# Performance work log

Measured on AMD Instinct MI355X. Metric: run time of the kernel, lower is better.

Reference implementation:

```python
import jax, jax.numpy as jnp
import numpy as np

TOPK_FRAC = 0.2

def _l2norm(v, eps=1e-12):
    return v / (jnp.linalg.norm(v) + eps)

def _spectral_normalize(w, u):
    # torch.nn.utils.spectral_norm forward: one power iteration (u,v detached),
    # sigma = u^T W v with gradient flowing through W only.
    wm = w.reshape(w.shape[0], -1)            # (out, in*kh*kw)
    v = _l2norm(jax.lax.stop_gradient(wm).T @ u)
    u_new = _l2norm(jax.lax.stop_gradient(wm) @ v)
    sigma = jnp.einsum('i,ij,j->', u_new, wm, v)
    return w / sigma

def setup_inputs() -> dict:
    key = jax.random.key(0)
    ks = jax.random.split(key, 5)
    N, C, H, W = 32, 512, 56, 56
    return {
        'x':  jax.random.normal(ks[0], (N, C, H, W), dtype=jnp.float32),
        'w1': jax.random.normal(ks[1], (C, C, 4, 4), dtype=jnp.float32) * 0.05,
        'w2': jax.random.normal(ks[2], (C, C, 1, 1), dtype=jnp.float32) * 0.05,
        'u1': jax.random.normal(ks[3], (C,), dtype=jnp.float32),
        'u2': jax.random.normal(ks[4], (C,), dtype=jnp.float32),
    }

def reference(x, w1, w2, u1, u2):
    N, C, H, W = x.shape
    # AdaptiveAvgPool2d(4): H,W divisible by 4 -> uniform 14x14 windows
    p = x.reshape(N, C, 4, H // 4, 4, W // 4).mean(axis=(3, 5))   # (N,C,4,4)
    p = jax.nn.sigmoid(p)
    # spectral-norm conv 4x4, valid, no bias -> fully reduces spatial to 1x1
    w1n = _spectral_normalize(w1, u1)                             # (C,C,4,4)
    h = jnp.einsum('ncij,ocij->no', p, w1n)                       # (N,C)
    h = jax.nn.relu(h)
    # spectral-norm conv 1x1
    w2n = _spectral_normalize(w2, u2).reshape(C, C)               # (out,in)
    s = jax.nn.sigmoid(jnp.einsum('nc,oc->no', h, w2n))           # (N,C)
    # sparse_ch: keep top int(0.2*C) channels per sample
    k = int(max(1, TOPK_FRAC * C))
    _, idx = jax.lax.top_k(s, k)                                  # (N,k)
    mask = jnp.zeros_like(s).at[jnp.arange(N)[:, None], idx].set(1.0)
    weight = (s * mask)[:, :, None, None]                         # (N,C,1,1)
    return x * weight
```

## Files before the change

kernel.cpp:

```cpp
#include <hip/hip_runtime.h>


#define KTOP 102

__device__ __forceinline__ float block_sum256(float v) {
  __shared__ float red[4];
  #pragma unroll
  for (int off = 32; off; off >>= 1) v += __shfl_down(v, off, 64);
  int lane = threadIdx.x & 63;
  int w = threadIdx.x >> 6;
  if (lane == 0) red[w] = v;
  __syncthreads();
  float r = 0.f;
  if (threadIdx.x == 0) r = red[0] + red[1] + red[2] + red[3];
  return r;
}

__global__ __launch_bounds__(256) void k_pool(const float* __restrict__ x, float* __restrict__ p) {
  __shared__ float sx[3136];
  int plane = blockIdx.x;
  const float* xp = x + (size_t)plane * 3136;
  for (int e = threadIdx.x; e < 3136; e += 256) sx[e] = xp[e];
  __syncthreads();
  int t = threadIdx.x;
  int w = t >> 4, lane = t & 15;
  int wr = w >> 2, wc = w & 3;
  float acc = 0.f;
  for (int e = lane; e < 196; e += 16) {
    int r = e / 14, cc = e - r * 14;
    acc += sx[(14 * wr + r) * 56 + 14 * wc + cc];
  }
  #pragma unroll
  for (int off = 8; off; off >>= 1) acc += __shfl_down(acc, off, 16);
  if (lane == 0) {
    float m = acc * (1.f / 196.f);
    p[(size_t)plane * 16 + w] = 1.f / (1.f + expf(-m));
  }
}

__global__ __launch_bounds__(256) void k_sn1(const float* __restrict__ w1, const float* __restrict__ w2,
                                             const float* __restrict__ u1, const float* __restrict__ u2,
                                             float* __restrict__ part1, float* __restrict__ part1b) {
  __shared__ float su[64];
  int b = blockIdx.x, t = threadIdx.x;
  if (b < 256) {
    int jb = b & 31, ic = b >> 5;
    if (t < 64) su[t] = u1[ic * 64 + t];
    __syncthreads();
    int j = jb * 256 + t;
    const float* base = w1 + (size_t)(ic * 64) * 8192 + j;
    float acc = 0.f;
    #pragma unroll 4
    for (int i = 0; i < 64; ++i) acc += base[(size_t)i * 8192] * su[i];
    part1[ic * 8192 + j] = acc;
  } else {
    int bb = b - 256;
    int jb = bb & 1, ic = bb >> 1;
    if (t < 64) su[t] = u2[ic * 64 + t];
    __syncthreads();
    int j = jb * 256 + t;
    const float* base = w2 + (size_t)(ic * 64) * 512 + j;
    float acc = 0.f;
    #pragma unroll 4
    for (int i = 0; i < 64; ++i) acc += base[(size_t)i * 512] * su[i];
    part1b[ic * 512 + j] = acc;
  }
}

__global__ __launch_bounds__(256) void k_sn1r(const float* __restrict__ part1, const float* __restrict__ part1b,
                                              float* __restrict__ t1, float* __restrict__ t1b,
                                              float* __restrict__ scal) {
  int b = blockIdx.x, t = threadIdx.x;
  float s = 0.f;
  if (b < 32) {
    int j = b * 256 + t;
    #pragma unroll
    for (int ic = 0; ic < 8; ++ic) s += part1[ic * 8192 + j];
    t1[j] = s;
    float tot = block_sum256(s * s);
    if (t == 0) atomicAdd(&scal[0], tot);
  } else {
    int j = (b - 32) * 256 + t;
    #pragma unroll
    for (int ic = 0; ic < 8; ++ic) s += part1b[ic * 512 + j];
    t1b[j] = s;
    float tot = block_sum256(s * s);
    if (t == 0) atomicAdd(&scal[1], tot);
  }
}

__global__ __launch_bounds__(256) void k_sn2(const float* __restrict__ w1, const float* __restrict__ w2,
                                             const float* __restrict__ t1, const float* __restrict__ t1b,
                                             float* __restrict__ scal) {
  int b = blockIdx.x, t = threadIdx.x;
  if (b < 512) {
    float inv = 1.f / (sqrtf(scal[0]) + 1e-12f);
    const float4* row = (const float4*)(w1 + (size_t)b * 8192);
    const float4* tv = (const float4*)t1;
    float acc = 0.f;
    for (int q = t; q < 2048; q += 256) {
      float4 a = row[q], v = tv[q];
      acc += a.x * v.x + a.y * v.y + a.z * v.z + a.w * v.w;
    }
    float tot = block_sum256(acc);
    if (t == 0) { float r = tot * inv; atomicAdd(&scal[2], r * r); }
  } else {
    int i = b - 512;
    float inv = 1.f / (sqrtf(scal[1]) + 1e-12f);
    const float4* row = (const float4*)(w2 + (size_t)i * 512);
    const float4* tv = (const float4*)t1b;
    float acc = 0.f;
    if (t < 128) {
      float4 a = row[t], v = tv[t];
      acc = a.x * v.x + a.y * v.y + a.z * v.z + a.w * v.w;
    }
    float tot = block_sum256(acc);
    if (t == 0) { float r = tot * inv; atomicAdd(&scal[3], r * r); }
  }
}

__global__ __launch_bounds__(256) void k_gemm1(const float* __restrict__ p, const float* __restrict__ w1,
                                               float* __restrict__ part) {
  __shared__ float sp[32][132];
  __shared__ float sw[64][132];
  int t = threadIdx.x;
  int o0 = blockIdx.x * 64;
  int k0 = blockIdx.y * 128;
  for (int idx = t; idx < 32 * 128; idx += 256) {
    int r = idx >> 7, c = idx & 127;
    sp[r][c] = p[(size_t)r * 8192 + k0 + c];
  }
  for (int idx = t; idx < 64 * 128; idx += 256) {
    int r = idx >> 7, c = idx & 127;
    sw[r][c] = w1[(size_t)(o0 + r) * 8192 + k0 + c];
  }
  __syncthreads();
  int m = t & 31, g = t >> 5;
  int n0 = g * 4;
  float acc[4][2] = {{0.f, 0.f}, {0.f, 0.f}, {0.f, 0.f}, {0.f, 0.f}};
  for (int kk = 0; kk < 128; kk += 4) {
    float4 wa = *(const float4*)&sw[m][kk];
    float4 wb = *(const float4*)&sw[m + 32][kk];
    #pragma unroll
    for (int ni = 0; ni < 4; ++ni) {
      float4 pv = *(const float4*)&sp[n0 + ni][kk];
      acc[ni][0] += pv.x * wa.x + pv.y * wa.y + pv.z * wa.z + pv.w * wa.w;
      acc[ni][1] += pv.x * wb.x + pv.y * wb.y + pv.z * wb.z + pv.w * wb.w;
    }
  }
  size_t base = (size_t)blockIdx.y * 16384;
  #pragma unroll
  for (int ni = 0; ni < 4; ++ni) {
    part[base + (n0 + ni) * 512 + o0 + m] = acc[ni][0];
    part[base + (n0 + ni) * 512 + o0 + m + 32] = acc[ni][1];
  }
}

__global__ __launch_bounds__(256) void k_hred(const float* __restrict__ part, const float* __restrict__ scal,
                                              float* __restrict__ h) {
  int idx = blockIdx.x * 256 + threadIdx.x;
  float s = 0.f;
  for (int ks = 0; ks < 64; ++ks) s += part[(size_t)ks * 16384 + idx];
  float A2 = scal[2];
  float sigma = A2 / (sqrtf(A2) + 1e-12f);
  h[idx] = fmaxf(s / sigma, 0.f);
}

__global__ __launch_bounds__(256) void k_gemm2_topk(const float* __restrict__ h, const float* __restrict__ w2,
                                                    const float* __restrict__ scal, float* __restrict__ wgt) {
  __shared__ float sh[512];
  __shared__ float ss[512];
  __shared__ unsigned sb[512];
  __shared__ int cnt;
  int n = blockIdx.x, t = threadIdx.x;
  sh[t] = h[n * 512 + t];
  sh[t + 256] = h[n * 512 + t + 256];
  __syncthreads();
  float B2 = scal[3];
  float inv_sigma = (sqrtf(B2) + 1e-12f) / B2;
  {
    int o0 = t, o1 = t + 256;
    const float4* r0 = (const float4*)(w2 + (size_t)o0 * 512);
    const float4* r1 = (const float4*)(w2 + (size_t)o1 * 512);
    float d0 = 0.f, d1 = 0.f;
    for (int q = 0; q < 128; ++q) {
      float4 hv = *(const float4*)&sh[q * 4];
      float4 a = r0[q], b = r1[q];
      d0 += hv.x * a.x + hv.y * a.y + hv.z * a.z + hv.w * a.w;
      d1 += hv.x * b.x + hv.y * b.y + hv.z * b.z + hv.w * b.w;
    }
    float s0 = 1.f / (1.f + expf(-d0 * inv_sigma));
    float s1 = 1.f / (1.f + expf(-d1 * inv_sigma));
    ss[o0] = s0; ss[o1] = s1;
    sb[o0] = __float_as_uint(s0); sb[o1] = __float_as_uint(s1);
  }
  __syncthreads();
  int r = KTOP;
  unsigned prefix = 0u;
  for (int bit = 31; bit >= 0; --bit) {
    if (t == 0) cnt = 0;
    __syncthreads();
    unsigned hi = prefix | (1u << bit);
    unsigned mhi = ~((1u << bit) - 1u);
    bool m0 = (sb[t] & mhi) == hi;
    bool m1 = (sb[t + 256] & mhi) == hi;
    unsigned long long c0 = __ballot(m0);
    unsigned long long c1 = __ballot(m1);
    if ((t & 63) == 0) atomicAdd(&cnt, __popcll(c0) + __popcll(c1));
    __syncthreads();
    int c = cnt;
    __syncthreads();
    if (c >= r) prefix = hi; else r -= c;
  }
  if (t == 0) cnt = 0;
  __syncthreads();
  {
    unsigned long long g0 = __ballot(sb[t] > prefix);
    unsigned long long g1 = __ballot(sb[t + 256] > prefix);
    if ((t & 63) == 0) atomicAdd(&cnt, __popcll(g0) + __popcll(g1));
  }
  __syncthreads();
  int alloweq = KTOP - cnt;
  for (int e = t; e < 512; e += 256) {
    unsigned v = sb[e];
    bool keep = v > prefix;
    if (!keep && v == prefix) {
      int rank = 0;
      for (int j = 0; j < e; ++j) rank += (sb[j] == prefix);
      keep = rank < alloweq;
    }
    wgt[n * 512 + e] = keep ? ss[e] : 0.f;
  }
}

__global__ __launch_bounds__(256) void k_scale(const float* __restrict__ x, const float* __restrict__ wgt,
                                               float* __restrict__ out) {
  int plane = blockIdx.x;
  float g = wgt[plane];
  const float4* xi = (const float4*)(x + (size_t)plane * 3136);
  float4* oo = (float4*)(out + (size_t)plane * 3136);
  for (int e = threadIdx.x; e < 784; e += 256) {
    float4 v = xi[e];
    v.x *= g; v.y *= g; v.z *= g; v.w *= g;
    oo[e] = v;
  }
}

extern "C" void kernel_launch(void* const* d_in, const int* in_sizes, int n_in,
                              void* d_out, int out_size, void* d_ws, size_t ws_size,
                              hipStream_t stream) {
  const float* x  = (const float*)d_in[0];
  const float* w1 = (const float*)d_in[1];
  const float* w2 = (const float*)d_in[2];
  const float* u1 = (const float*)d_in[3];
  const float* u2 = (const float*)d_in[4];
  float* out = (float*)d_out;
  float* ws = (float*)d_ws;

  float* scal   = ws + 0;
  float* t1     = ws + 4;
  float* t1b    = ws + 8196;
  float* p      = ws + 8708;
  float* part1  = ws + 270852;
  float* part1b = ws + 336388;
  float* part   = ws + 340484;
  float* h      = ws + 1389060;
  float* wgt    = ws + 1405444;

  (void)hipMemsetAsync(scal, 0, 16, stream);
  k_pool<<<16384, 256, 0, stream>>>(x, p);
  k_sn1<<<272, 256, 0, stream>>>(w1, w2, u1, u2, part1, part1b);
  k_sn1r<<<34, 256, 0, stream>>>(part1, part1b, t1, t1b, scal);
  k_sn2<<<1024, 256, 0, stream>>>(w1, w2, t1, t1b, scal);
  k_gemm1<<<dim3(8, 64), 256, 0, stream>>>(p, w1, part);
  k_hred<<<64, 256, 0, stream>>>(part, scal, h);
  k_gemm2_topk<<<32, 256, 0, stream>>>(h, w2, scal, wgt);
  k_scale<<<16384, 256, 0, stream>>>(x, wgt, out);
}
```

Measured before the change: 512.2 us.

## Merge independent stages into shared launches and split gemm2 from top-k

```diff
diff --git a/kernel.cpp b/kernel.cpp
--- a/kernel.cpp
+++ b/kernel.cpp
@@ -16,35 +16,36 @@
   return r;
 }
 
-__global__ __launch_bounds__(256) void k_pool(const float* __restrict__ x, float* __restrict__ p) {
+__global__ __launch_bounds__(256) void k_a(const float* __restrict__ x, const float* __restrict__ w1,
+                                           const float* __restrict__ w2, const float* __restrict__ u1,
+                                           const float* __restrict__ u2, float* __restrict__ p,
+                                           float* __restrict__ part1, float* __restrict__ part1b,
+                                           float* __restrict__ scal) {
   __shared__ float sx[3136];
-  int plane = blockIdx.x;
-  const float* xp = x + (size_t)plane * 3136;
-  for (int e = threadIdx.x; e < 3136; e += 256) sx[e] = xp[e];
-  __syncthreads();
-  int t = threadIdx.x;
-  int w = t >> 4, lane = t & 15;
-  int wr = w >> 2, wc = w & 3;
-  float acc = 0.f;
-  for (int e = lane; e < 196; e += 16) {
-    int r = e / 14, cc = e - r * 14;
-    acc += sx[(14 * wr + r) * 56 + 14 * wc + cc];
-  }
-  #pragma unroll
-  for (int off = 8; off; off >>= 1) acc += __shfl_down(acc, off, 16);
-  if (lane == 0) {
-    float m = acc * (1.f / 196.f);
-    p[(size_t)plane * 16 + w] = 1.f / (1.f + expf(-m));
-  }
-}
-
-__global__ __launch_bounds__(256) void k_sn1(const float* __restrict__ w1, const float* __restrict__ w2,
-                                             const float* __restrict__ u1, const float* __restrict__ u2,
-                                             float* __restrict__ part1, float* __restrict__ part1b) {
   __shared__ float su[64];
   int b = blockIdx.x, t = threadIdx.x;
-  if (b < 256) {
-    int jb = b & 31, ic = b >> 5;
+  if (b < 16384) {
+    const float4* xp4 = (const float4*)(x + (size_t)b * 3136);
+    float4* sx4 = (float4*)sx;
+    for (int e = t; e < 784; e += 256) sx4[e] = xp4[e];
+    __syncthreads();
+    int w = t >> 4, lane = t & 15;
+    int wr = w >> 2, wc = w & 3;
+    float acc = 0.f;
+    for (int e = lane; e < 196; e += 16) {
+      int r = e / 14, cc = e - r * 14;
+      acc += sx[(14 * wr + r) * 56 + 14 * wc + cc];
+    }
+    #pragma unroll
+    for (int off = 8; off; off >>= 1) acc += __shfl_down(acc, off, 16);
+    if (lane == 0) {
+      float m = acc * (1.f / 196.f);
+      p[(size_t)b * 16 + w] = 1.f / (1.f + expf(-m));
+    }
+  } else if (b < 16640) {
+    int bb = b - 16384;
+    if (bb == 0 && t < 4) scal[t] = 0.f;
+    int jb = bb & 31, ic = bb >> 5;
     if (t < 64) su[t] = u1[ic * 64 + t];
     __syncthreads();
     int j = jb * 256 + t;
@@ -54,7 +55,7 @@
     for (int i = 0; i < 64; ++i) acc += base[(size_t)i * 8192] * su[i];
     part1[ic * 8192 + j] = acc;
   } else {
-    int bb = b - 256;
+    int bb = b - 16640;
     int jb = bb & 1, ic = bb >> 1;
     if (t < 64) su[t] = u2[ic * 64 + t];
     __syncthreads();
@@ -67,20 +68,55 @@
   }
 }
 
-__global__ __launch_bounds__(256) void k_sn1r(const float* __restrict__ part1, const float* __restrict__ part1b,
-                                              float* __restrict__ t1, float* __restrict__ t1b,
-                                              float* __restrict__ scal) {
+__global__ __launch_bounds__(256) void k_b(const float* __restrict__ p, const float* __restrict__ w1,
+                                           const float* __restrict__ part1, const float* __restrict__ part1b,
+                                           float* __restrict__ part, float* __restrict__ t1,
+                                           float* __restrict__ t1b, float* __restrict__ scal) {
+  __shared__ float sp[32][132];
+  __shared__ float sw[64][132];
   int b = blockIdx.x, t = threadIdx.x;
-  float s = 0.f;
-  if (b < 32) {
-    int j = b * 256 + t;
+  if (b < 512) {
+    int o0 = (b & 7) * 64;
+    int k0 = (b >> 3) * 128;
+    for (int idx = t; idx < 1024; idx += 256) {
+      int r = idx >> 5, c4 = (idx & 31) << 2;
+      *(float4*)&sp[r][c4] = *(const float4*)&p[(size_t)r * 8192 + k0 + c4];
+    }
+    for (int idx = t; idx < 2048; idx += 256) {
+      int r = idx >> 5, c4 = (idx & 31) << 2;
+      *(float4*)&sw[r][c4] = *(const float4*)&w1[(size_t)(o0 + r) * 8192 + k0 + c4];
+    }
+    __syncthreads();
+    int m = t & 31, g = t >> 5;
+    int n0 = g * 4;
+    float acc[4][2] = {{0.f, 0.f}, {0.f, 0.f}, {0.f, 0.f}, {0.f, 0.f}};
+    for (int kk = 0; kk < 128; kk += 4) {
+      float4 wa = *(const float4*)&sw[m][kk];
+      float4 wb = *(const float4*)&sw[m + 32][kk];
+      #pragma unroll
+      for (int ni = 0; ni < 4; ++ni) {
+        float4 pv = *(const float4*)&sp[n0 + ni][kk];
+        acc[ni][0] += pv.x * wa.x + pv.y * wa.y + pv.z * wa.z + pv.w * wa.w;
+        acc[ni][1] += pv.x * wb.x + pv.y * wb.y + pv.z * wb.z + pv.w * wb.w;
+      }
+    }
+    size_t base = (size_t)(b >> 3) * 16384;
+    #pragma unroll
+    for (int ni = 0; ni < 4; ++ni) {
+      part[base + (n0 + ni) * 512 + o0 + m] = acc[ni][0];
+      part[base + (n0 + ni) * 512 + o0 + m + 32] = acc[ni][1];
+    }
+  } else if (b < 544) {
+    int j = (b - 512) * 256 + t;
+    float s = 0.f;
     #pragma unroll
     for (int ic = 0; ic < 8; ++ic) s += part1[ic * 8192 + j];
     t1[j] = s;
     float tot = block_sum256(s * s);
     if (t == 0) atomicAdd(&scal[0], tot);
   } else {
-    int j = (b - 32) * 256 + t;
+    int j = (b - 544) * 256 + t;
+    float s = 0.f;
     #pragma unroll
     for (int ic = 0; ic < 8; ++ic) s += part1b[ic * 512 + j];
     t1b[j] = s;
@@ -89,13 +125,20 @@
   }
 }
 
-__global__ __launch_bounds__(256) void k_sn2(const float* __restrict__ w1, const float* __restrict__ w2,
-                                             const float* __restrict__ t1, const float* __restrict__ t1b,
-                                             float* __restrict__ scal) {
+__global__ __launch_bounds__(256) void k_c(const float* __restrict__ part, const float* __restrict__ w1,
+                                           const float* __restrict__ w2, const float* __restrict__ t1,
+                                           const float* __restrict__ t1b, float* __restrict__ h,
+                                           float* __restrict__ scal) {
   int b = blockIdx.x, t = threadIdx.x;
-  if (b < 512) {
+  if (b < 64) {
+    int idx = b * 256 + t;
+    float s = 0.f;
+    for (int ks = 0; ks < 64; ++ks) s += part[(size_t)ks * 16384 + idx];
+    h[idx] = fmaxf(s, 0.f);
+  } else if (b < 576) {
+    int i = b - 64;
     float inv = 1.f / (sqrtf(scal[0]) + 1e-12f);
-    const float4* row = (const float4*)(w1 + (size_t)b * 8192);
+    const float4* row = (const float4*)(w1 + (size_t)i * 8192);
     const float4* tv = (const float4*)t1;
     float acc = 0.f;
     for (int q = t; q < 2048; q += 256) {
@@ -105,7 +148,7 @@
     float tot = block_sum256(acc);
     if (t == 0) { float r = tot * inv; atomicAdd(&scal[2], r * r); }
   } else {
-    int i = b - 512;
+    int i = b - 576;
     float inv = 1.f / (sqrtf(scal[1]) + 1e-12f);
     const float4* row = (const float4*)(w2 + (size_t)i * 512);
     const float4* tv = (const float4*)t1b;
@@ -119,81 +162,38 @@
   }
 }
 
-__global__ __launch_bounds__(256) void k_gemm1(const float* __restrict__ p, const float* __restrict__ w1,
-                                               float* __restrict__ part) {
-  __shared__ float sp[32][132];
-  __shared__ float sw[64][132];
-  int t = threadIdx.x;
-  int o0 = blockIdx.x * 64;
-  int k0 = blockIdx.y * 128;
-  for (int idx = t; idx < 32 * 128; idx += 256) {
-    int r = idx >> 7, c = idx & 127;
-    sp[r][c] = p[(size_t)r * 8192 + k0 + c];
-  }
-  for (int idx = t; idx < 64 * 128; idx += 256) {
-    int r = idx >> 7, c = idx & 127;
-    sw[r][c] = w1[(size_t)(o0 + r) * 8192 + k0 + c];
-  }
-  __syncthreads();
-  int m = t & 31, g = t >> 5;
-  int n0 = g * 4;
-  float acc[4][2] = {{0.f, 0.f}, {0.f, 0.f}, {0.f, 0.f}, {0.f, 0.f}};
-  for (int kk = 0; kk < 128; kk += 4) {
-    float4 wa = *(const float4*)&sw[m][kk];
-    float4 wb = *(const float4*)&sw[m + 32][kk];
-    #pragma unroll
-    for (int ni = 0; ni < 4; ++ni) {
-      float4 pv = *(const float4*)&sp[n0 + ni][kk];
-      acc[ni][0] += pv.x * wa.x + pv.y * wa.y + pv.z * wa.z + pv.w * wa.w;
-      acc[ni][1] += pv.x * wb.x + pv.y * wb.y + pv.z * wb.z + pv.w * wb.w;
-    }
-  }
-  size_t base = (size_t)blockIdx.y * 16384;
+__global__ __launch_bounds__(256) void k_gemm2(const float* __restrict__ h, const float* __restrict__ w2,
+                                               const float* __restrict__ scal, float* __restrict__ s_out) {
+  int o = blockIdx.x, t = threadIdx.x;
+  int w = t >> 6, lane = t & 63;
+  float A2 = scal[2], B2 = scal[3];
+  float sig1 = A2 / (sqrtf(A2) + 1e-12f);
+  float sig2 = B2 / (sqrtf(B2) + 1e-12f);
+  float inv = 1.f / (sig1 * sig2);
+  const float4* wr = (const float4*)(w2 + (size_t)o * 512);
+  float4 wa = wr[lane * 2], wb = wr[lane * 2 + 1];
   #pragma unroll
-  for (int ni = 0; ni < 4; ++ni) {
-    part[base + (n0 + ni) * 512 + o0 + m] = acc[ni][0];
-    part[base + (n0 + ni) * 512 + o0 + m + 32] = acc[ni][1];
-  }
-}
-
-__global__ __launch_bounds__(256) void k_hred(const float* __restrict__ part, const float* __restrict__ scal,
-                                              float* __restrict__ h) {
-  int idx = blockIdx.x * 256 + threadIdx.x;
-  float s = 0.f;
-  for (int ks = 0; ks < 64; ++ks) s += part[(size_t)ks * 16384 + idx];
-  float A2 = scal[2];
-  float sigma = A2 / (sqrtf(A2) + 1e-12f);
-  h[idx] = fmaxf(s / sigma, 0.f);
-}
-
-__global__ __launch_bounds__(256) void k_gemm2_topk(const float* __restrict__ h, const float* __restrict__ w2,
-                                                    const float* __restrict__ scal, float* __restrict__ wgt) {
-  __shared__ float sh[512];
+  for (int j = 0; j < 8; ++j) {
+    int n = w * 8 + j;
+    const float4* hr = (const float4*)(h + (size_t)n * 512);
+    float4 ha = hr[lane * 2], hb = hr[lane * 2 + 1];
+    float d = ha.x * wa.x + ha.y * wa.y + ha.z * wa.z + ha.w * wa.w
+            + hb.x * wb.x + hb.y * wb.y + hb.z * wb.z + hb.w * wb.w;
+    #pragma unroll
+    for (int off = 32; off; off >>= 1) d += __shfl_down(d, off, 64);
+    if (lane == 0) s_out[(size_t)n * 512 + o] = 1.f / (1.f + expf(-d * inv));
+  }
+}
+
+__global__ __launch_bounds__(256) void k_topk(const float* __restrict__ s_in, float* __restrict__ wgt) {
   __shared__ float ss[512];
   __shared__ unsigned sb[512];
   __shared__ int cnt;
   int n = blockIdx.x, t = threadIdx.x;
-  sh[t] = h[n * 512 + t];
-  sh[t + 256] = h[n * 512 + t + 256];
-  __syncthreads();
-  float B2 = scal[3];
-  float inv_sigma = (sqrtf(B2) + 1e-12f) / B2;
-  {
-    int o0 = t, o1 = t + 256;
-    const float4* r0 = (const float4*)(w2 + (size_t)o0 * 512);
-    const float4* r1 = (const float4*)(w2 + (size_t)o1 * 512);
-    float d0 = 0.f, d1 = 0.f;
-    for (int q = 0; q < 128; ++q) {
-      float4 hv = *(const float4*)&sh[q * 4];
-      float4 a = r0[q], b = r1[q];
-      d0 += hv.x * a.x + hv.y * a.y + hv.z * a.z + hv.w * a.w;
-      d1 += hv.x * b.x + hv.y * b.y + hv.z * b.z + hv.w * b.w;
-    }
-    float s0 = 1.f / (1.f + expf(-d0 * inv_sigma));
-    float s1 = 1.f / (1.f + expf(-d1 * inv_sigma));
-    ss[o0] = s0; ss[o1] = s1;
-    sb[o0] = __float_as_uint(s0); sb[o1] = __float_as_uint(s1);
-  }
+  float v0 = s_in[(size_t)n * 512 + t];
+  float v1 = s_in[(size_t)n * 512 + 256 + t];
+  ss[t] = v0; ss[t + 256] = v1;
+  sb[t] = __float_as_uint(v0); sb[t + 256] = __float_as_uint(v1);
   __syncthreads();
   int r = KTOP;
   unsigned prefix = 0u;
@@ -202,10 +202,8 @@
     __syncthreads();
     unsigned hi = prefix | (1u << bit);
     unsigned mhi = ~((1u << bit) - 1u);
-    bool m0 = (sb[t] & mhi) == hi;
-    bool m1 = (sb[t + 256] & mhi) == hi;
-    unsigned long long c0 = __ballot(m0);
-    unsigned long long c1 = __ballot(m1);
+    unsigned long long c0 = __ballot((sb[t] & mhi) == hi);
+    unsigned long long c1 = __ballot((sb[t + 256] & mhi) == hi);
     if ((t & 63) == 0) atomicAdd(&cnt, __popcll(c0) + __popcll(c1));
     __syncthreads();
     int c = cnt;
@@ -229,7 +227,7 @@
       for (int j = 0; j < e; ++j) rank += (sb[j] == prefix);
       keep = rank < alloweq;
     }
-    wgt[n * 512 + e] = keep ? ss[e] : 0.f;
+    wgt[(size_t)n * 512 + e] = keep ? ss[e] : 0.f;
   }
 }
 
@@ -265,15 +263,13 @@
   float* part1b = ws + 336388;
   float* part   = ws + 340484;
   float* h      = ws + 1389060;
-  float* wgt    = ws + 1405444;
-
-  (void)hipMemsetAsync(scal, 0, 16, stream);
-  k_pool<<<16384, 256, 0, stream>>>(x, p);
-  k_sn1<<<272, 256, 0, stream>>>(w1, w2, u1, u2, part1, part1b);
-  k_sn1r<<<34, 256, 0, stream>>>(part1, part1b, t1, t1b, scal);
-  k_sn2<<<1024, 256, 0, stream>>>(w1, w2, t1, t1b, scal);
-  k_gemm1<<<dim3(8, 64), 256, 0, stream>>>(p, w1, part);
-  k_hred<<<64, 256, 0, stream>>>(part, scal, h);
-  k_gemm2_topk<<<32, 256, 0, stream>>>(h, w2, scal, wgt);
+  float* s      = ws + 1405444;
+  float* wgt    = ws + 1421828;
+
+  k_a<<<16656, 256, 0, stream>>>(x, w1, w2, u1, u2, p, part1, part1b, scal);
+  k_b<<<546, 256, 0, stream>>>(p, w1, part1, part1b, part, t1, t1b, scal);
+  k_c<<<1088, 256, 0, stream>>>(part, w1, w2, t1, t1b, h, scal);
+  k_gemm2<<<512, 256, 0, stream>>>(h, w2, scal, s);
+  k_topk<<<32, 256, 0, stream>>>(s, wgt);
   k_scale<<<16384, 256, 0, stream>>>(x, wgt, out);
 }
```

New measurement: 457.6 us. -10.7%, faster.
